# Performance work log

Hardware: AMD Instinct MI355X
Metric: run time of the kernel (lower is better)

The kernel has to match this reference:

```python
import jax, jax.numpy as jnp
import numpy as np

NUM_STREAM = 4
SINKHORN_ITERS = 20
HC_EPS = 1e-06
NORM_EPS = 1e-06


def sinkhorn_knopps(h, iters, eps):
    # h: [B, S, ns, ns]
    h = jax.nn.softmax(h, axis=-1) + eps
    h = h / (h.sum(-2, keepdims=True) + eps)
    for _ in range(iters - 1):  # fixed small trip count (19), unrolled
        h = h / (h.sum(-1, keepdims=True) + eps)
        h = h / (h.sum(-2, keepdims=True) + eps)
    return h


def setup_inputs() -> dict:
    key = jax.random.key(0)
    k1, k2, k3, k4 = jax.random.split(key, 4)
    B, S, ns, H = 4, 2048, NUM_STREAM, 1024
    mix_hc = (2 + ns) * ns  # 24
    x = jax.random.normal(k1, (B, S, ns, H), dtype=jnp.float32)
    hc_fn = jax.random.normal(k2, (mix_hc, ns * H), dtype=jnp.float32) * 0.02
    hc_scale = jax.random.uniform(k3, (3,), dtype=jnp.float32)
    hc_base = jax.random.normal(k4, (mix_hc,), dtype=jnp.float32)
    return {"x": x, "hc_fn": hc_fn, "hc_scale": hc_scale, "hc_base": hc_base}


def reference(x, hc_fn, hc_scale, hc_base):
    B, S, ns, H = x.shape
    xf = x.reshape(B, S, ns * H).astype(jnp.float32)
    # RMSNorm stats (applied as a post-scale on the linear output, as in source)
    rsqrt = jax.lax.rsqrt(jnp.mean(jnp.square(xf), axis=-1, keepdims=True) + NORM_EPS)
    weight = jnp.einsum('bsd,md->bsm', xf, hc_fn) * rsqrt  # [B, S, mix_hc]
    h_pre = weight[..., :ns]
    h_post = weight[..., ns:2 * ns]
    h_res = weight[..., 2 * ns:].reshape(B, S, ns, ns)
    h_pre = jax.nn.sigmoid(h_pre * hc_scale[0] + hc_base[:ns][None, None, :]) + HC_EPS
    h_post = 2.0 * jax.nn.sigmoid(h_post * hc_scale[1] + hc_base[ns:2 * ns][None, None, :])
    h_res = h_res * hc_scale[2] + hc_base[2 * ns:].reshape(ns, ns)[None, None, :, :]
    h_res = sinkhorn_knopps(h_res, SINKHORN_ITERS, HC_EPS)
    xs = xf.reshape(B, S, ns, H)
    # hc_pre: mix streams into a single vector per token
    y = jnp.einsum('bsn,bsnh->bsh', h_pre, xs)  # [B, S, H]
    # hc_post: broadcast gated y back to streams + Sinkhorn-mixed residual streams
    out = h_post[..., None] * y[:, :, None, :] + jnp.einsum('bsij,bsih->bsjh', h_res, xs)
    return out.astype(x.dtype)
```

## Files before the change

### kernel.cpp

```cpp
#include <hip/hip_runtime.h>
#include <math.h>

#define NS 4
#define HDIM 1024
#define DDIM 4096
#define MT 16
#define KCH 512
#define HC_EPS_F 1e-6f
#define NORM_EPS_F 1e-6f

typedef __attribute__((ext_vector_type(8))) short short8;
typedef __attribute__((ext_vector_type(4))) float f32x4;

__device__ __forceinline__ float frcp(float v) { return __builtin_amdgcn_rcpf(v); }

#define CVT_PAIR(j, f0, f1)                                                     \
  { unsigned p0 = __float_as_uint(f0), p1 = __float_as_uint(f1);                \
    H.u[j] = (p1 & 0xFFFF0000u) | (p0 >> 16);                                   \
    unsigned q0 = __float_as_uint((f0) - __uint_as_float(p0 & 0xFFFF0000u));    \
    unsigned q1 = __float_as_uint((f1) - __uint_as_float(p1 & 0xFFFF0000u));    \
    L.u[j] = (q1 & 0xFFFF0000u) | (q0 >> 16); }

__device__ __forceinline__ void cvt_hl(const float4 a, const float4 b,
                                       short8& hi, short8& lo) {
  union { unsigned u[4]; short8 s; } H, L;
  CVT_PAIR(0, a.x, a.y)
  CVT_PAIR(1, a.z, a.w)
  CVT_PAIR(2, b.x, b.y)
  CVT_PAIR(3, b.z, b.w)
  hi = H.s; lo = L.s;
}

__launch_bounds__(256, 2)
__global__ void mhc_dots_mfma(const float* __restrict__ x,
                              const float* __restrict__ hc_fn,
                              float* __restrict__ w,
                              float* __restrict__ sq) {
  const int lane = threadIdx.x & 63;
  const int wave = threadIdx.x >> 6;
  const int wunit = blockIdx.x * 4 + wave;
  const int mt = wunit >> 3;
  const int kc = wunit & 7;
  const long long tok0 = (long long)mt * MT;
  const int k0 = kc * KCH;

  const int row = lane & 15;
  const int ks  = lane >> 4;

  const float4* ap  = (const float4*)(x + (tok0 + row) * DDIM + k0) + ks * 2;
  const float4* bp0 = (const float4*)(hc_fn + (long long)row * DDIM + k0) + ks * 2;
  const int fr1c = (row < 8) ? (16 + row) : 23;
  const float4* bp1 = (const float4*)(hc_fn + (long long)fr1c * DDIM + k0) + ks * 2;
  const bool v1 = (row < 8);
  const float4 z4 = {0.f, 0.f, 0.f, 0.f};

  f32x4 acc0 = {0.f, 0.f, 0.f, 0.f};
  f32x4 acc1 = {0.f, 0.f, 0.f, 0.f};
  float ssq = 0.f;

  float4 ca0 = ap[0],  ca1 = ap[1];
  float4 cb00 = bp0[0], cb01 = bp0[1];
  float4 cb10 = v1 ? bp1[0] : z4, cb11 = v1 ? bp1[1] : z4;

  #pragma unroll 2
  for (int s = 0; s < KCH / 32; ++s) {
    float4 na0, na1, nb00, nb01, nb10, nb11;
    if (s < 15) {
      const int o = (s + 1) * 8;
      na0 = ap[o]; na1 = ap[o + 1];
      nb00 = bp0[o]; nb01 = bp0[o + 1];
      nb10 = v1 ? bp1[o] : z4; nb11 = v1 ? bp1[o + 1] : z4;
    }

    ssq = fmaf(ca0.x, ca0.x, fmaf(ca0.y, ca0.y, fmaf(ca0.z, ca0.z, fmaf(ca0.w, ca0.w, ssq))));
    ssq = fmaf(ca1.x, ca1.x, fmaf(ca1.y, ca1.y, fmaf(ca1.z, ca1.z, fmaf(ca1.w, ca1.w, ssq))));

    short8 ahi, alo, b0hi, b0lo, b1hi, b1lo;
    cvt_hl(ca0, ca1, ahi, alo);
    cvt_hl(cb00, cb01, b0hi, b0lo);
    cvt_hl(cb10, cb11, b1hi, b1lo);

    acc0 = __builtin_amdgcn_mfma_f32_16x16x32_bf16(ahi, b0hi, acc0, 0, 0, 0);
    acc1 = __builtin_amdgcn_mfma_f32_16x16x32_bf16(ahi, b1hi, acc1, 0, 0, 0);
    acc0 = __builtin_amdgcn_mfma_f32_16x16x32_bf16(ahi, b0lo, acc0, 0, 0, 0);
    acc1 = __builtin_amdgcn_mfma_f32_16x16x32_bf16(ahi, b1lo, acc1, 0, 0, 0);
    acc0 = __builtin_amdgcn_mfma_f32_16x16x32_bf16(alo, b0hi, acc0, 0, 0, 0);
    acc1 = __builtin_amdgcn_mfma_f32_16x16x32_bf16(alo, b1hi, acc1, 0, 0, 0);

    if (s < 15) {
      ca0 = na0; ca1 = na1;
      cb00 = nb00; cb01 = nb01;
      cb10 = nb10; cb11 = nb11;
    }
  }

  ssq += __shfl_xor(ssq, 16, 64);
  ssq += __shfl_xor(ssq, 32, 64);
  if (lane < 16) atomicAdd(&sq[tok0 + lane], ssq);

  const int rq = lane >> 4;
  #pragma unroll
  for (int r = 0; r < 4; ++r)
    atomicAdd(&w[(tok0 + rq * 4 + r) * 24 + row], acc0[r]);
  if (row < 8) {
    #pragma unroll
    for (int r = 0; r < 4; ++r)
      atomicAdd(&w[(tok0 + rq * 4 + r) * 24 + 16 + row], acc1[r]);
  }
}

__launch_bounds__(256, 4)
__global__ void mhc_sinkhorn(float* __restrict__ w,
                             const float* __restrict__ sq,
                             const float* __restrict__ hc_scale,
                             const float* __restrict__ hc_base) {
  const int lane = threadIdx.x & 63;
  const int wave = threadIdx.x >> 6;
  const long long tok = (long long)blockIdx.x * 16 + wave * 4 + (lane >> 4);
  const int e = lane & 15;

  float* wt = w + tok * 24;
  const float rs = rsqrtf(sq[tok] * (1.0f / DDIM) + NORM_EPS_F);
  const float s0 = hc_scale[0], s1 = hc_scale[1], s2 = hc_scale[2];

  float h = wt[8 + e] * rs * s2 + hc_base[8 + e];
  float mx = fmaxf(h, __shfl_xor(h, 1, 4));
  mx = fmaxf(mx, __shfl_xor(mx, 2, 4));
  float ex = expf(h - mx);
  float sm = ex + __shfl_xor(ex, 1, 4);
  sm += __shfl_xor(sm, 2, 4);
  h = ex * frcp(sm) + HC_EPS_F;
  float cs = h + __shfl_xor(h, 4, 16);
  cs += __shfl_xor(cs, 8, 16);
  h *= frcp(cs + HC_EPS_F);
  #pragma unroll 1
  for (int itn = 0; itn < 19; ++itn) {
    float rsum = h + __shfl_xor(h, 1, 4);
    rsum += __shfl_xor(rsum, 2, 4);
    h *= frcp(rsum + HC_EPS_F);
    float csum = h + __shfl_xor(h, 4, 16);
    csum += __shfl_xor(csum, 8, 16);
    h *= frcp(csum + HC_EPS_F);
  }
  float gp = 0.f, gq = 0.f;
  if (e < NS) {
    gp = frcp(1.0f + expf(-(wt[e] * rs * s0 + hc_base[e]))) + HC_EPS_F;
    gq = 2.0f * frcp(1.0f + expf(-(wt[NS + e] * rs * s1 + hc_base[NS + e])));
  }
  wt[8 + e] = h;
  if (e < NS) { wt[e] = gp; wt[NS + e] = gq; }
}

__launch_bounds__(256, 8)
__global__ void mhc_out(const float* __restrict__ x,
                        const float* __restrict__ gates,
                        float* __restrict__ out) {
  const long long token = blockIdx.x;
  const int q = threadIdx.x;

  const float* g = gates + token * 24;
  float hp[NS], hq[NS], hr[NS][NS];
  #pragma unroll
  for (int i = 0; i < NS; ++i) {
    hp[i] = g[i];
    hq[i] = g[NS + i];
    #pragma unroll
    for (int j = 0; j < NS; ++j) hr[i][j] = g[8 + i * NS + j];
  }

  const float4* xb = (const float4*)(x + token * DDIM);
  float4 xv[NS];
  #pragma unroll
  for (int i = 0; i < NS; ++i) xv[i] = xb[i * 256 + q];

  float4 y;
  y.x = hp[0]*xv[0].x + hp[1]*xv[1].x + hp[2]*xv[2].x + hp[3]*xv[3].x;
  y.y = hp[0]*xv[0].y + hp[1]*xv[1].y + hp[2]*xv[2].y + hp[3]*xv[3].y;
  y.z = hp[0]*xv[0].z + hp[1]*xv[1].z + hp[2]*xv[2].z + hp[3]*xv[3].z;
  y.w = hp[0]*xv[0].w + hp[1]*xv[1].w + hp[2]*xv[2].w + hp[3]*xv[3].w;

  float4* ob = (float4*)(out + token * DDIM);
  #pragma unroll
  for (int n = 0; n < NS; ++n) {
    float4 o;
    o.x = hq[n]*y.x + hr[0][n]*xv[0].x + hr[1][n]*xv[1].x + hr[2][n]*xv[2].x + hr[3][n]*xv[3].x;
    o.y = hq[n]*y.y + hr[0][n]*xv[0].y + hr[1][n]*xv[1].y + hr[2][n]*xv[2].y + hr[3][n]*xv[3].y;
    o.z = hq[n]*y.z + hr[0][n]*xv[0].z + hr[1][n]*xv[1].z + hr[2][n]*xv[2].z + hr[3][n]*xv[3].z;
    o.w = hq[n]*y.w + hr[0][n]*xv[0].w + hr[1][n]*xv[1].w + hr[2][n]*xv[2].w + hr[3][n]*xv[3].w;
    ob[n * 256 + q] = o;
  }
}

extern "C" void kernel_launch(void* const* d_in, const int* in_sizes, int n_in,
                              void* d_out, int out_size, void* d_ws, size_t ws_size,
                              hipStream_t stream) {
  const float* x        = (const float*)d_in[0];
  const float* hc_fn    = (const float*)d_in[1];
  const float* hc_scale = (const float*)d_in[2];
  const float* hc_base  = (const float*)d_in[3];
  float* out = (float*)d_out;

  const int ntok = in_sizes[0] / DDIM;
  float* w  = (float*)d_ws;
  float* sq = out;

  hipMemsetAsync(w, 0, (size_t)ntok * 24 * sizeof(float), stream);
  hipMemsetAsync(sq, 0, (size_t)ntok * sizeof(float), stream);

  const int wave_units = (ntok / MT) * 8;
  mhc_dots_mfma<<<wave_units / 4, 256, 0, stream>>>(x, hc_fn, w, sq);
  mhc_sinkhorn<<<ntok / 16, 256, 0, stream>>>(w, sq, hc_scale, hc_base);
  mhc_out<<<ntok, 256, 0, stream>>>(x, w, out);
}
```

Baseline: 98.50 us.

## Replace atomic accumulation with per-chunk partial buffers and deepen prefetch

The dots kernel now writes per-K-chunk partial sums (weights plus sum of squares) into a scratch region carved out of the output buffer, instead of issuing atomicAdds into zeroed workspace. The sinkhorn kernel reduces the 8 partials per token itself, which removes both memsets and the atomic traffic. The load pipeline is deepened to prefetch two steps ahead, and launch bounds are relaxed to one block per SIMD for more registers. The trade-off is extra partial-buffer reads in the sinkhorn kernel and possibly lower occupancy in the dots kernel.

```diff
diff --git a/kernel.cpp b/kernel.cpp
--- a/kernel.cpp
+++ b/kernel.cpp
@@ -6,6 +6,7 @@
 #define DDIM 4096
 #define MT 16
 #define KCH 512
+#define NKC 8
 #define HC_EPS_F 1e-6f
 #define NORM_EPS_F 1e-6f
 
@@ -31,11 +32,10 @@
   hi = H.s; lo = L.s;
 }
 
-__launch_bounds__(256, 2)
+__launch_bounds__(256, 1)
 __global__ void mhc_dots_mfma(const float* __restrict__ x,
                               const float* __restrict__ hc_fn,
-                              float* __restrict__ w,
-                              float* __restrict__ sq) {
+                              float* __restrict__ wp, int ntok) {
   const int lane = threadIdx.x & 63;
   const int wave = threadIdx.x >> 6;
   const int wunit = blockIdx.x * 4 + wave;
@@ -58,27 +58,30 @@
   f32x4 acc1 = {0.f, 0.f, 0.f, 0.f};
   float ssq = 0.f;
 
-  float4 ca0 = ap[0],  ca1 = ap[1];
-  float4 cb00 = bp0[0], cb01 = bp0[1];
-  float4 cb10 = v1 ? bp1[0] : z4, cb11 = v1 ? bp1[1] : z4;
-
-  #pragma unroll 2
+  float4 a0_c = ap[0], a1_c = ap[1];
+  float4 b00_c = bp0[0], b01_c = bp0[1];
+  float4 b10_c = v1 ? bp1[0] : z4, b11_c = v1 ? bp1[1] : z4;
+  float4 a0_n = ap[8], a1_n = ap[9];
+  float4 b00_n = bp0[8], b01_n = bp0[9];
+  float4 b10_n = v1 ? bp1[8] : z4, b11_n = v1 ? bp1[9] : z4;
+
+  #pragma unroll 4
   for (int s = 0; s < KCH / 32; ++s) {
-    float4 na0, na1, nb00, nb01, nb10, nb11;
-    if (s < 15) {
-      const int o = (s + 1) * 8;
-      na0 = ap[o]; na1 = ap[o + 1];
-      nb00 = bp0[o]; nb01 = bp0[o + 1];
-      nb10 = v1 ? bp1[o] : z4; nb11 = v1 ? bp1[o + 1] : z4;
+    float4 a0_p, a1_p, b00_p, b01_p, b10_p, b11_p;
+    if (s < 14) {
+      const int o = (s + 2) * 8;
+      a0_p = ap[o]; a1_p = ap[o + 1];
+      b00_p = bp0[o]; b01_p = bp0[o + 1];
+      b10_p = v1 ? bp1[o] : z4; b11_p = v1 ? bp1[o + 1] : z4;
     }
 
-    ssq = fmaf(ca0.x, ca0.x, fmaf(ca0.y, ca0.y, fmaf(ca0.z, ca0.z, fmaf(ca0.w, ca0.w, ssq))));
-    ssq = fmaf(ca1.x, ca1.x, fmaf(ca1.y, ca1.y, fmaf(ca1.z, ca1.z, fmaf(ca1.w, ca1.w, ssq))));
+    ssq = fmaf(a0_c.x, a0_c.x, fmaf(a0_c.y, a0_c.y, fmaf(a0_c.z, a0_c.z, fmaf(a0_c.w, a0_c.w, ssq))));
+    ssq = fmaf(a1_c.x, a1_c.x, fmaf(a1_c.y, a1_c.y, fmaf(a1_c.z, a1_c.z, fmaf(a1_c.w, a1_c.w, ssq))));
 
     short8 ahi, alo, b0hi, b0lo, b1hi, b1lo;
-    cvt_hl(ca0, ca1, ahi, alo);
-    cvt_hl(cb00, cb01, b0hi, b0lo);
-    cvt_hl(cb10, cb11, b1hi, b1lo);
+    cvt_hl(a0_c, a1_c, ahi, alo);
+    cvt_hl(b00_c, b01_c, b0hi, b0lo);
+    cvt_hl(b10_c, b11_c, b1hi, b1lo);
 
     acc0 = __builtin_amdgcn_mfma_f32_16x16x32_bf16(ahi, b0hi, acc0, 0, 0, 0);
     acc1 = __builtin_amdgcn_mfma_f32_16x16x32_bf16(ahi, b1hi, acc1, 0, 0, 0);
@@ -88,42 +91,58 @@
     acc1 = __builtin_amdgcn_mfma_f32_16x16x32_bf16(alo, b1hi, acc1, 0, 0, 0);
 
     if (s < 15) {
-      ca0 = na0; ca1 = na1;
-      cb00 = nb00; cb01 = nb01;
-      cb10 = nb10; cb11 = nb11;
+      a0_c = a0_n; a1_c = a1_n;
+      b00_c = b00_n; b01_c = b01_n;
+      b10_c = b10_n; b11_c = b11_n;
+    }
+    if (s < 14) {
+      a0_n = a0_p; a1_n = a1_p;
+      b00_n = b00_p; b01_n = b01_p;
+      b10_n = b10_p; b11_n = b11_p;
     }
   }
 
   ssq += __shfl_xor(ssq, 16, 64);
   ssq += __shfl_xor(ssq, 32, 64);
-  if (lane < 16) atomicAdd(&sq[tok0 + lane], ssq);
-
+
+  float* wpk = wp + (long long)kc * ntok * 25;
+  if (lane < 16) wpk[(tok0 + lane) * 25 + 24] = ssq;
   const int rq = lane >> 4;
   #pragma unroll
   for (int r = 0; r < 4; ++r)
-    atomicAdd(&w[(tok0 + rq * 4 + r) * 24 + row], acc0[r]);
+    wpk[(tok0 + rq * 4 + r) * 25 + row] = acc0[r];
   if (row < 8) {
     #pragma unroll
     for (int r = 0; r < 4; ++r)
-      atomicAdd(&w[(tok0 + rq * 4 + r) * 24 + 16 + row], acc1[r]);
+      wpk[(tok0 + rq * 4 + r) * 25 + 16 + row] = acc1[r];
   }
 }
 
 __launch_bounds__(256, 4)
-__global__ void mhc_sinkhorn(float* __restrict__ w,
-                             const float* __restrict__ sq,
+__global__ void mhc_sinkhorn(const float* __restrict__ wp,
                              const float* __restrict__ hc_scale,
-                             const float* __restrict__ hc_base) {
+                             const float* __restrict__ hc_base,
+                             float* __restrict__ gates, int ntok) {
   const int lane = threadIdx.x & 63;
   const int wave = threadIdx.x >> 6;
   const long long tok = (long long)blockIdx.x * 16 + wave * 4 + (lane >> 4);
   const int e = lane & 15;
 
-  float* wt = w + tok * 24;
-  const float rs = rsqrtf(sq[tok] * (1.0f / DDIM) + NORM_EPS_F);
+  const long long kstride = (long long)ntok * 25;
+  const float* b = wp + tok * 25;
+  float sres = 0.f, ssq = 0.f, spre = 0.f, spost = 0.f;
+  #pragma unroll
+  for (int kc = 0; kc < NKC; ++kc) {
+    const float* p = b + kc * kstride;
+    sres += p[8 + e];
+    ssq  += p[24];
+    if (e < NS) { spre += p[e]; spost += p[NS + e]; }
+  }
+
+  const float rs = rsqrtf(ssq * (1.0f / DDIM) + NORM_EPS_F);
   const float s0 = hc_scale[0], s1 = hc_scale[1], s2 = hc_scale[2];
 
-  float h = wt[8 + e] * rs * s2 + hc_base[8 + e];
+  float h = sres * rs * s2 + hc_base[8 + e];
   float mx = fmaxf(h, __shfl_xor(h, 1, 4));
   mx = fmaxf(mx, __shfl_xor(mx, 2, 4));
   float ex = expf(h - mx);
@@ -142,13 +161,12 @@
     csum += __shfl_xor(csum, 8, 16);
     h *= frcp(csum + HC_EPS_F);
   }
-  float gp = 0.f, gq = 0.f;
+  float* g = gates + tok * 24;
+  g[8 + e] = h;
   if (e < NS) {
-    gp = frcp(1.0f + expf(-(wt[e] * rs * s0 + hc_base[e]))) + HC_EPS_F;
-    gq = 2.0f * frcp(1.0f + expf(-(wt[NS + e] * rs * s1 + hc_base[NS + e])));
-  }
-  wt[8 + e] = h;
-  if (e < NS) { wt[e] = gp; wt[NS + e] = gq; }
+    g[e] = frcp(1.0f + expf(-(spre * rs * s0 + hc_base[e]))) + HC_EPS_F;
+    g[NS + e] = 2.0f * frcp(1.0f + expf(-(spost * rs * s1 + hc_base[NS + e])));
+  }
 }
 
 __launch_bounds__(256, 8)
@@ -201,14 +219,11 @@
   float* out = (float*)d_out;
 
   const int ntok = in_sizes[0] / DDIM;
-  float* w  = (float*)d_ws;
-  float* sq = out;
-
-  hipMemsetAsync(w, 0, (size_t)ntok * 24 * sizeof(float), stream);
-  hipMemsetAsync(sq, 0, (size_t)ntok * sizeof(float), stream);
-
-  const int wave_units = (ntok / MT) * 8;
-  mhc_dots_mfma<<<wave_units / 4, 256, 0, stream>>>(x, hc_fn, w, sq);
-  mhc_sinkhorn<<<ntok / 16, 256, 0, stream>>>(w, sq, hc_scale, hc_base);
-  mhc_out<<<ntok, 256, 0, stream>>>(x, w, out);
-}
+  float* gates = (float*)d_ws;
+  float* wp    = out;
+
+  const int wave_units = (ntok / MT) * NKC;
+  mhc_dots_mfma<<<wave_units / 4, 256, 0, stream>>>(x, hc_fn, wp, ntok);
+  mhc_sinkhorn<<<ntok / 16, 256, 0, stream>>>(wp, hc_scale, hc_base, gates, ntok);
+  mhc_out<<<ntok, 256, 0, stream>>>(x, gates, out);
+}
```

Result: faster. 95.18 us (-3.4%).
